# Optimization experiments

Measured on AMD Instinct MI355X. Metric: run time of the kernel, lower is better.

## Reference

```python
import jax, jax.numpy as jnp
import numpy as np

N_NODES = 50000
N_EDGES = 600000
CH = 128      # units / channels
RBF = 200     # ceil(cutoff/gap) = ceil(20.0/0.1)
LOG2 = 0.6931471805599453


def shifted_softplus(x):
    # tf.where(x < 14, softplus(where(x < 14, x, 0)), x) - log(2)
    safe = jnp.where(x < 14.0, x, jnp.zeros_like(x))
    return jnp.where(x < 14.0, jax.nn.softplus(safe), x) - LOG2


def _glorot(key, shape):
    fan_in = shape[0] if len(shape) > 1 else shape[0]
    fan_out = shape[-1]
    lim = np.sqrt(6.0 / (fan_in + fan_out))
    return jax.random.uniform(key, shape, jnp.float32, -lim, lim)


def setup_inputs() -> dict:
    key = jax.random.key(0)
    ks = jax.random.split(key, 12)
    rbf = jax.random.uniform(ks[0], (N_EDGES, RBF), jnp.float32)
    x = jax.random.normal(ks[1], (N_NODES, CH), jnp.float32)
    src = jax.random.randint(ks[2], (N_EDGES,), 0, N_NODES, jnp.int32)
    return {
        "rbf": rbf,
        "x": x,
        "src": src,
        "w1": _glorot(ks[3], (RBF, CH)),
        "b1": _glorot(ks[4], (CH,)),
        "w2": _glorot(ks[5], (CH, CH)),
        "b2": _glorot(ks[6], (CH,)),
        "w3": _glorot(ks[7], (CH, CH)),
        "w4": _glorot(ks[8], (CH, CH)),
        "b4": _glorot(ks[9], (CH,)),
        "w5": _glorot(ks[10], (CH, CH)),
        "b5": _glorot(ks[11], (CH,)),
    }


def reference(rbf, x, src, w1, b1, w2, b2, w3, w4, b4, w5, b5):
    # filter-generating MLP on edge RBF features: [E, RBF] -> [E, CH]
    h = shifted_softplus(rbf @ w1 + b1)
    w = shifted_softplus(h @ w2 + b2)
    # node feature transform, gather to edges by SOURCE index
    f = x @ w3                         # [N, CH]
    wf = w * f[src]                    # [E, CH] broadcast_node_to_edges + multiply
    # scatter-sum edges back to SOURCE nodes
    conv = jax.ops.segment_sum(wf, src, num_segments=N_NODES)  # [N, CH]
    # output MLP + residual
    y = shifted_softplus(conv @ w4 + b4)
    v = y @ w5 + b5
    return x + v
```

## Files before the change

### kernel.cpp

```cpp
#include <hip/hip_runtime.h>

#define CH      128
#define RBFD    200
#define NNODES  50000
#define NEDGES  600000
#define LOG2F_  0.6931471805599453f
#define K1P     224

typedef __attribute__((ext_vector_type(8))) __bf16 bf16x8;
typedef __attribute__((ext_vector_type(4))) float  f32x4;

__device__ __forceinline__ float ssp(float x) {
    float sp = (x < 14.0f) ? __logf(1.0f + __expf(x)) : x;
    return sp - LOG2F_;
}

__device__ __forceinline__ unsigned short f2bf(float f) {
    union { float f; unsigned int u; } v; v.f = f;
    unsigned int r = v.u + 0x7FFFu + ((v.u >> 16) & 1u);
    return (unsigned short)(r >> 16);
}

__device__ __forceinline__ float bf2f(unsigned short s) {
    union { unsigned int u; float f; } v; v.u = ((unsigned int)s) << 16;
    return v.f;
}

__device__ __forceinline__ bf16x8 load_cvt8(const float* p) {
    float4 f0 = *(const float4*)p;
    float4 f1 = *(const float4*)(p + 4);
    union { unsigned int u[4]; bf16x8 v; } r;
    asm("v_cvt_pk_bf16_f32 %0, %1, %2" : "=v"(r.u[0]) : "v"(f0.x), "v"(f0.y));
    asm("v_cvt_pk_bf16_f32 %0, %1, %2" : "=v"(r.u[1]) : "v"(f0.z), "v"(f0.w));
    asm("v_cvt_pk_bf16_f32 %0, %1, %2" : "=v"(r.u[2]) : "v"(f1.x), "v"(f1.y));
    asm("v_cvt_pk_bf16_f32 %0, %1, %2" : "=v"(r.u[3]) : "v"(f1.z), "v"(f1.w));
    return r.v;
}

__global__ __launch_bounds__(256) void prep_weights(const float* __restrict__ w1,
                                                    const float* __restrict__ w2,
                                                    unsigned short* __restrict__ w1T,
                                                    unsigned short* __restrict__ w2T) {
    int i = blockIdx.x * 256 + threadIdx.x;
    if (i < 128 * K1P) {
        int n = i / K1P, k = i % K1P;
        w1T[i] = (k < RBFD) ? f2bf(w1[k * CH + n]) : (unsigned short)0;
    } else {
        int j = i - 128 * K1P;
        if (j < 128 * 128) {
            int n = j / 128, k = j % 128;
            w2T[j] = f2bf(w2[k * CH + n]);
        }
    }
}

__global__ __launch_bounds__(256) void k_hist(const int* __restrict__ src, int* __restrict__ cur) {
    int e = blockIdx.x * 256 + threadIdx.x;
    if (e < NEDGES) atomicAdd(&cur[src[e]], 1);
}

__global__ __launch_bounds__(256) void k_scan1(const int* __restrict__ cur, int* __restrict__ bsum) {
    __shared__ int s[256];
    const int t = threadIdx.x;
    int i = blockIdx.x * 256 + t;
    s[t] = (i < NNODES) ? cur[i] : 0;
    __syncthreads();
    for (int d = 128; d > 0; d >>= 1) {
        if (t < d) s[t] += s[t + d];
        __syncthreads();
    }
    if (t == 0) bsum[blockIdx.x] = s[0];
}

__global__ __launch_bounds__(256) void k_scan2(const int* __restrict__ bsum, int* __restrict__ bpre) {
    __shared__ int s[256];
    const int t = threadIdx.x;
    int v0 = (t < 196) ? bsum[t] : 0;
    s[t] = v0;
    __syncthreads();
    for (int d = 1; d < 256; d <<= 1) {
        int v = (t >= d) ? s[t - d] : 0;
        __syncthreads();
        s[t] += v;
        __syncthreads();
    }
    if (t < 196) bpre[t] = s[t] - v0;
}

__global__ __launch_bounds__(256) void k_scan3(const int* __restrict__ deg_in,
                                               const int* __restrict__ bpre,
                                               int* __restrict__ csr_off,
                                               int* __restrict__ cur) {
    __shared__ int s[256];
    const int t = threadIdx.x, b = blockIdx.x;
    const int i = b * 256 + t;
    int d0 = (i < NNODES) ? deg_in[i] : 0;
    s[t] = d0;
    __syncthreads();
    for (int d = 1; d < 256; d <<= 1) {
        int v = (t >= d) ? s[t - d] : 0;
        __syncthreads();
        s[t] += v;
        __syncthreads();
    }
    if (i < NNODES) {
        int ex = bpre[b] + s[t] - d0;
        csr_off[i] = ex;
        cur[i] = ex;
    }
    if (i == NNODES - 1) csr_off[NNODES] = NEDGES;
}

__global__ __launch_bounds__(256) void k_fill(const int* __restrict__ src,
                                              int* __restrict__ cur,
                                              int* __restrict__ eidx) {
    int e = blockIdx.x * 256 + threadIdx.x;
    if (e < NEDGES) {
        int pos = atomicAdd(&cur[src[e]], 1);
        eidx[pos] = e;
    }
}

__global__ __launch_bounds__(256, 4) void edge_kernel2(const float* __restrict__ rbf,
                                                       const float* __restrict__ b1v,
                                                       const float* __restrict__ b2v,
                                                       const unsigned short* __restrict__ w1T,
                                                       const unsigned short* __restrict__ w2T,
                                                       unsigned short* __restrict__ wbuf) {
    __shared__ unsigned short tile[4][16 * 128];
    const int t = threadIdx.x;
    const int lane = t & 63;
    const int wv = t >> 6;
    const int l15 = lane & 15;
    const int lg  = lane >> 4;
    const size_t erow0 = (size_t)blockIdx.x * 64 + (size_t)wv * 16;
    unsigned short* my = tile[wv];
    char* myb = (char*)my;

    bf16x8 a1[7];
    const float* arow = rbf + (erow0 + l15) * RBFD;
#pragma unroll
    for (int kt = 0; kt < 6; kt++)
        a1[kt] = load_cvt8(arow + kt * 32 + lg * 8);
    if (lg == 0) {
        a1[6] = load_cvt8(arow + 192);
    } else {
        union { unsigned int u[4]; bf16x8 v; } z;
        z.u[0] = z.u[1] = z.u[2] = z.u[3] = 0;
        a1[6] = z.v;
    }

    const int myrow0 = lg * 4;

#pragma unroll
    for (int nt = 0; nt < 8; nt++) {
        f32x4 acc = {0.f, 0.f, 0.f, 0.f};
        const unsigned short* bbase = w1T + (size_t)(nt * 16 + l15) * K1P + lg * 8;
#pragma unroll
        for (int kt = 0; kt < 7; kt++) {
            bf16x8 b = *(const bf16x8*)(bbase + kt * 32);
            acc = __builtin_amdgcn_mfma_f32_16x16x32_bf16(a1[kt], b, acc, 0, 0, 0);
        }
        const float bias = b1v[nt * 16 + l15];
#pragma unroll
        for (int r = 0; r < 4; r++) {
            const int row = myrow0 + r;
            const int colb = (nt * 32 + l15 * 2) ^ ((row & 7) << 4);
            *(unsigned short*)(myb + row * 256 + colb) = f2bf(ssp(acc[r] + bias));
        }
    }

    bf16x8 a2[4];
#pragma unroll
    for (int kt = 0; kt < 4; kt++) {
        const int boff = l15 * 256 + ((kt * 64 + lg * 16) ^ ((l15 & 7) << 4));
        a2[kt] = *(const bf16x8*)(myb + boff);
    }

#pragma unroll
    for (int nt = 0; nt < 8; nt++) {
        f32x4 acc = {0.f, 0.f, 0.f, 0.f};
        const unsigned short* bbase = w2T + (size_t)(nt * 16 + l15) * 128 + lg * 8;
#pragma unroll
        for (int kt = 0; kt < 4; kt++) {
            bf16x8 b = *(const bf16x8*)(bbase + kt * 32);
            acc = __builtin_amdgcn_mfma_f32_16x16x32_bf16(a2[kt], b, acc, 0, 0, 0);
        }
        const float bias = b2v[nt * 16 + l15];
#pragma unroll
        for (int r = 0; r < 4; r++) {
            const int row = myrow0 + r;
            const int colb = (nt * 32 + l15 * 2) ^ ((row & 7) << 4);
            *(unsigned short*)(myb + row * 256 + colb) = f2bf(ssp(acc[r] + bias));
        }
    }

    {
        const int row = lane >> 2, q = lane & 3;
        float4 o[4];
#pragma unroll
        for (int j = 0; j < 4; j++) {
            const int boff = row * 256 + ((q * 64 + j * 16) ^ ((row & 7) << 4));
            o[j] = *(const float4*)(myb + boff);
        }
        float4* gdst = (float4*)((char*)wbuf + (erow0 + row) * 256 + q * 64);
#pragma unroll
        for (int j = 0; j < 4; j++) gdst[j] = o[j];
    }
}

__global__ __launch_bounds__(256) void node_gather2(const float* __restrict__ x,
                                                    const float* __restrict__ w3,
                                                    const float* __restrict__ w4,
                                                    const float* __restrict__ b4,
                                                    const float* __restrict__ w5,
                                                    const float* __restrict__ b5,
                                                    const unsigned short* __restrict__ wbuf,
                                                    const int* __restrict__ eidx,
                                                    const int* __restrict__ csr_off,
                                                    float* __restrict__ out,
                                                    int n_nodes) {
    __shared__ float A[32 * 128];
    __shared__ float B[32 * 128];
    const int t = threadIdx.x;
    const int n0 = blockIdx.x * 32;
    const int rows = min(32, n_nodes - n0);

    {
        const float4* g = (const float4*)(x + (size_t)n0 * CH);
        float4* s = (float4*)A;
        for (int i = t; i < rows * 32; i += 256) s[i] = g[i];
    }
    __syncthreads();

    const int c = t & 127, eh = t >> 7;
    float acc[16];

#pragma unroll
    for (int i = 0; i < 16; i++) acc[i] = 0.f;
    for (int k = 0; k < 128; k += 4) {
        const float wa = w3[(k + 0) * CH + c];
        const float wb = w3[(k + 1) * CH + c];
        const float wc = w3[(k + 2) * CH + c];
        const float wd = w3[(k + 3) * CH + c];
#pragma unroll
        for (int i = 0; i < 16; i++) {
            const float4 v = *(const float4*)&A[(eh * 16 + i) * CH + k];
            acc[i] = fmaf(v.x, wa, acc[i]);
            acc[i] = fmaf(v.y, wb, acc[i]);
            acc[i] = fmaf(v.z, wc, acc[i]);
            acc[i] = fmaf(v.w, wd, acc[i]);
        }
    }
#pragma unroll
    for (int i = 0; i < 16; i++) B[(eh * 16 + i) * 128 + c] = acc[i];
    __syncthreads();

    {
        const int lane = t & 63, wv = t >> 6;
        const int c0 = lane * 2;
        for (int rr = 0; rr < 8; rr++) {
            const int r = wv * 8 + rr;
            const int n = n0 + r;
            float s0 = 0.f, s1 = 0.f;
            if (n < n_nodes) {
                const int o0 = csr_off[n], o1 = csr_off[n + 1];
                int j = o0;
                for (; j + 3 < o1; j += 4) {
                    const int ea = eidx[j], eb = eidx[j + 1], ec = eidx[j + 2], ed = eidx[j + 3];
                    const unsigned ua = *(const unsigned*)(wbuf + (size_t)ea * CH + c0);
                    const unsigned ub = *(const unsigned*)(wbuf + (size_t)eb * CH + c0);
                    const unsigned uc = *(const unsigned*)(wbuf + (size_t)ec * CH + c0);
                    const unsigned ud = *(const unsigned*)(wbuf + (size_t)ed * CH + c0);
                    s0 += bf2f((unsigned short)ua) + bf2f((unsigned short)ub)
                        + bf2f((unsigned short)uc) + bf2f((unsigned short)ud);
                    s1 += bf2f((unsigned short)(ua >> 16)) + bf2f((unsigned short)(ub >> 16))
                        + bf2f((unsigned short)(uc >> 16)) + bf2f((unsigned short)(ud >> 16));
                }
                for (; j < o1; j++) {
                    const unsigned ua = *(const unsigned*)(wbuf + (size_t)eidx[j] * CH + c0);
                    s0 += bf2f((unsigned short)ua);
                    s1 += bf2f((unsigned short)(ua >> 16));
                }
            }
            const float2 f2 = *(const float2*)&B[r * 128 + c0];
            float2 v2;
            v2.x = (n < n_nodes) ? f2.x * s0 : 0.f;
            v2.y = (n < n_nodes) ? f2.y * s1 : 0.f;
            *(float2*)&B[r * 128 + c0] = v2;
        }
    }
    __syncthreads();

#pragma unroll
    for (int i = 0; i < 16; i++) acc[i] = 0.f;
    for (int k = 0; k < 128; k += 4) {
        const float wa = w4[(k + 0) * CH + c];
        const float wb = w4[(k + 1) * CH + c];
        const float wc = w4[(k + 2) * CH + c];
        const float wd = w4[(k + 3) * CH + c];
#pragma unroll
        for (int i = 0; i < 16; i++) {
            const float4 v = *(const float4*)&B[(eh * 16 + i) * CH + k];
            acc[i] = fmaf(v.x, wa, acc[i]);
            acc[i] = fmaf(v.y, wb, acc[i]);
            acc[i] = fmaf(v.z, wc, acc[i]);
            acc[i] = fmaf(v.w, wd, acc[i]);
        }
    }
    {
        const float bias4 = b4[c];
#pragma unroll
        for (int i = 0; i < 16; i++)
            A[(eh * 16 + i) * 128 + c] = ssp(acc[i] + bias4);
    }
    __syncthreads();

#pragma unroll
    for (int i = 0; i < 16; i++) acc[i] = 0.f;
    for (int k = 0; k < 128; k += 4) {
        const float wa = w5[(k + 0) * CH + c];
        const float wb = w5[(k + 1) * CH + c];
        const float wc = w5[(k + 2) * CH + c];
        const float wd = w5[(k + 3) * CH + c];
#pragma unroll
        for (int i = 0; i < 16; i++) {
            const float4 v = *(const float4*)&A[(eh * 16 + i) * CH + k];
            acc[i] = fmaf(v.x, wa, acc[i]);
            acc[i] = fmaf(v.y, wb, acc[i]);
            acc[i] = fmaf(v.z, wc, acc[i]);
            acc[i] = fmaf(v.w, wd, acc[i]);
        }
    }
    {
        const float bias5 = b5[c];
#pragma unroll
        for (int i = 0; i < 16; i++) {
            const int r = eh * 16 + i;
            if (r < rows) {
                const size_t off = ((size_t)(n0 + r)) * CH + c;
                out[off] = x[off] + acc[i] + bias5;
            }
        }
    }
}

static inline size_t align_up(size_t v, size_t a) { return (v + a - 1) & ~(a - 1); }

extern "C" void kernel_launch(void* const* d_in, const int* in_sizes, int n_in,
                              void* d_out, int out_size, void* d_ws, size_t ws_size,
                              hipStream_t stream) {
    const float* rbf = (const float*)d_in[0];
    const float* x   = (const float*)d_in[1];
    const int*   src = (const int*)d_in[2];
    const float* w1  = (const float*)d_in[3];
    const float* b1  = (const float*)d_in[4];
    const float* w2  = (const float*)d_in[5];
    const float* b2  = (const float*)d_in[6];
    const float* w3  = (const float*)d_in[7];
    const float* w4  = (const float*)d_in[8];
    const float* b4  = (const float*)d_in[9];
    const float* w5  = (const float*)d_in[10];
    const float* b5  = (const float*)d_in[11];

    float* out = (float*)d_out;
    const size_t wElems = 128 * K1P + 128 * 128;

    size_t off = 0;
    const size_t o_wbuf = off;  off = align_up(off + (size_t)NEDGES * CH * 2, 256);
    const size_t o_eidx = off;  off = align_up(off + (size_t)NEDGES * 4, 256);
    const size_t o_csr  = off;  off = align_up(off + (size_t)(NNODES + 1) * 4, 256);
    const size_t o_cur  = off;  off = align_up(off + (size_t)NNODES * 4, 256);
    const size_t o_bs   = off;  off = align_up(off + 256 * 4, 256);
    const size_t o_bp   = off;  off = align_up(off + 256 * 4, 256);
    const size_t o_wT   = off;  off = align_up(off + wElems * 2, 256);

    unsigned short* wbuf = (unsigned short*)((char*)d_ws + o_wbuf);
    int* eidx            = (int*)((char*)d_ws + o_eidx);
    int* csr_off         = (int*)((char*)d_ws + o_csr);
    int* cur             = (int*)((char*)d_ws + o_cur);
    int* bsum            = (int*)((char*)d_ws + o_bs);
    int* bpre            = (int*)((char*)d_ws + o_bp);
    unsigned short* w1T  = (unsigned short*)((char*)d_ws + o_wT);
    unsigned short* w2T  = w1T + 128 * K1P;

    hipMemsetAsync(cur, 0, (size_t)NNODES * 4, stream);
    prep_weights<<<(int)((wElems + 255) / 256), 256, 0, stream>>>(w1, w2, w1T, w2T);
    edge_kernel2<<<NEDGES / 64, 256, 0, stream>>>(rbf, b1, b2, w1T, w2T, wbuf);
    k_hist<<<(NEDGES + 255) / 256, 256, 0, stream>>>(src, cur);
    k_scan1<<<196, 256, 0, stream>>>(cur, bsum);
    k_scan2<<<1, 256, 0, stream>>>(bsum, bpre);
    k_scan3<<<196, 256, 0, stream>>>(cur, bpre, csr_off, cur);
    k_fill<<<(NEDGES + 255) / 256, 256, 0, stream>>>(src, cur, eidx);
    node_gather2<<<(NNODES + 31) / 32, 256, 0, stream>>>(x, w3, w4, b4, w5, b5,
                                                         wbuf, eidx, csr_off, out, NNODES);
}
```

Baseline: 593.0 us.

## Make edge MLP kernel persistent with weights staged in LDS

Rewrites the edge filter MLP as a persistent kernel of 256 blocks with 1024 threads. Each block copies padded bf16 W1/W2 (stride 232/136 to avoid bank conflicts) into shared memory once, then its waves pull 16-edge tiles through an atomic work counter. Weight B-operands come from LDS instead of global/L2, and biases are hoisted into registers. It also switches to a branchless softplus and uses the hardware bf16 convert instruction. The costs are a large LDS footprint (about 60 KB for weights plus 64 KB for tiles), which limits occupancy to one block per CU, and contention on the atomic counter.

```diff
diff --git a/kernel.cpp b/kernel.cpp
--- a/kernel.cpp
+++ b/kernel.cpp
@@ -4,14 +4,22 @@
 #define RBFD    200
 #define NNODES  50000
 #define NEDGES  600000
+#define NTILES  (NEDGES / 16)
 #define LOG2F_  0.6931471805599453f
-#define K1P     224
+
+#define W1STR   232
+#define W2STR   136
+#define W1ELEMS (128 * W1STR)
+#define W2ELEMS (128 * W2STR)
+#define WTOT    (W1ELEMS + W2ELEMS)
 
 typedef __attribute__((ext_vector_type(8))) __bf16 bf16x8;
 typedef __attribute__((ext_vector_type(4))) float  f32x4;
 
 __device__ __forceinline__ float ssp(float x) {
-    float sp = (x < 14.0f) ? __logf(1.0f + __expf(x)) : x;
+    float e  = __expf(x);
+    float sp = __logf(1.0f + e);
+    sp = (x < 14.0f) ? sp : x;
     return sp - LOG2F_;
 }
 
@@ -24,6 +32,12 @@
 __device__ __forceinline__ float bf2f(unsigned short s) {
     union { unsigned int u; float f; } v; v.u = ((unsigned int)s) << 16;
     return v.f;
+}
+
+__device__ __forceinline__ unsigned short cvt1bf(float f) {
+    unsigned int u;
+    asm("v_cvt_pk_bf16_f32 %0, %1, %2" : "=v"(u) : "v"(f), "v"(f));
+    return (unsigned short)u;
 }
 
 __device__ __forceinline__ bf16x8 load_cvt8(const float* p) {
@@ -39,18 +53,15 @@
 
 __global__ __launch_bounds__(256) void prep_weights(const float* __restrict__ w1,
                                                     const float* __restrict__ w2,
-                                                    unsigned short* __restrict__ w1T,
-                                                    unsigned short* __restrict__ w2T) {
+                                                    unsigned short* __restrict__ wp) {
     int i = blockIdx.x * 256 + threadIdx.x;
-    if (i < 128 * K1P) {
-        int n = i / K1P, k = i % K1P;
-        w1T[i] = (k < RBFD) ? f2bf(w1[k * CH + n]) : (unsigned short)0;
-    } else {
-        int j = i - 128 * K1P;
-        if (j < 128 * 128) {
-            int n = j / 128, k = j % 128;
-            w2T[j] = f2bf(w2[k * CH + n]);
-        }
+    if (i < W1ELEMS) {
+        int n = i / W1STR, k = i % W1STR;
+        wp[i] = (k < RBFD) ? f2bf(w1[k * CH + n]) : (unsigned short)0;
+    } else if (i < WTOT) {
+        int j = i - W1ELEMS;
+        int n = j / W2STR, k = j % W2STR;
+        wp[i] = (k < CH) ? f2bf(w2[k * CH + n]) : (unsigned short)0;
     }
 }
 
@@ -121,91 +132,112 @@
     }
 }
 
-__global__ __launch_bounds__(256, 4) void edge_kernel2(const float* __restrict__ rbf,
-                                                       const float* __restrict__ b1v,
-                                                       const float* __restrict__ b2v,
-                                                       const unsigned short* __restrict__ w1T,
-                                                       const unsigned short* __restrict__ w2T,
-                                                       unsigned short* __restrict__ wbuf) {
-    __shared__ unsigned short tile[4][16 * 128];
+__global__ __launch_bounds__(1024, 4) void edge_kernel3(const float* __restrict__ rbf,
+                                                        const float* __restrict__ b1v,
+                                                        const float* __restrict__ b2v,
+                                                        const unsigned short* __restrict__ wp,
+                                                        unsigned short* __restrict__ wbuf,
+                                                        int* __restrict__ ctr) {
+    __shared__ unsigned short wsh[WTOT];
+    __shared__ unsigned short htile[16 * 16 * 128];
     const int t = threadIdx.x;
     const int lane = t & 63;
-    const int wv = t >> 6;
+    const int wvid = t >> 6;
     const int l15 = lane & 15;
     const int lg  = lane >> 4;
-    const size_t erow0 = (size_t)blockIdx.x * 64 + (size_t)wv * 16;
-    unsigned short* my = tile[wv];
-    char* myb = (char*)my;
-
-    bf16x8 a1[7];
-    const float* arow = rbf + (erow0 + l15) * RBFD;
-#pragma unroll
-    for (int kt = 0; kt < 6; kt++)
-        a1[kt] = load_cvt8(arow + kt * 32 + lg * 8);
-    if (lg == 0) {
-        a1[6] = load_cvt8(arow + 192);
-    } else {
-        union { unsigned int u[4]; bf16x8 v; } z;
-        z.u[0] = z.u[1] = z.u[2] = z.u[3] = 0;
-        a1[6] = z.v;
-    }
-
+
+    {
+        const float4* g = (const float4*)wp;
+        float4* s = (float4*)wsh;
+        for (int i = t; i < WTOT / 8; i += 1024) s[i] = g[i];
+    }
+
+    float bias1[8], bias2[8];
+#pragma unroll
+    for (int nt = 0; nt < 8; nt++) {
+        bias1[nt] = b1v[nt * 16 + l15];
+        bias2[nt] = b2v[nt * 16 + l15];
+    }
+    __syncthreads();
+
+    const unsigned short* w1s = wsh;
+    const unsigned short* w2s = wsh + W1ELEMS;
+    char* myb = (char*)(htile + wvid * (16 * 128));
     const int myrow0 = lg * 4;
 
-#pragma unroll
-    for (int nt = 0; nt < 8; nt++) {
-        f32x4 acc = {0.f, 0.f, 0.f, 0.f};
-        const unsigned short* bbase = w1T + (size_t)(nt * 16 + l15) * K1P + lg * 8;
-#pragma unroll
-        for (int kt = 0; kt < 7; kt++) {
-            bf16x8 b = *(const bf16x8*)(bbase + kt * 32);
-            acc = __builtin_amdgcn_mfma_f32_16x16x32_bf16(a1[kt], b, acc, 0, 0, 0);
-        }
-        const float bias = b1v[nt * 16 + l15];
-#pragma unroll
-        for (int r = 0; r < 4; r++) {
-            const int row = myrow0 + r;
-            const int colb = (nt * 32 + l15 * 2) ^ ((row & 7) << 4);
-            *(unsigned short*)(myb + row * 256 + colb) = f2bf(ssp(acc[r] + bias));
-        }
-    }
-
-    bf16x8 a2[4];
-#pragma unroll
-    for (int kt = 0; kt < 4; kt++) {
-        const int boff = l15 * 256 + ((kt * 64 + lg * 16) ^ ((l15 & 7) << 4));
-        a2[kt] = *(const bf16x8*)(myb + boff);
-    }
-
-#pragma unroll
-    for (int nt = 0; nt < 8; nt++) {
-        f32x4 acc = {0.f, 0.f, 0.f, 0.f};
-        const unsigned short* bbase = w2T + (size_t)(nt * 16 + l15) * 128 + lg * 8;
+    while (true) {
+        int tile;
+        if (lane == 0) tile = atomicAdd(ctr, 1);
+        tile = __shfl(tile, 0);
+        if (tile >= NTILES) break;
+        const size_t erow0 = (size_t)tile * 16;
+
+        bf16x8 a1[7];
+        const float* arow = rbf + (erow0 + l15) * RBFD;
+#pragma unroll
+        for (int kt = 0; kt < 6; kt++)
+            a1[kt] = load_cvt8(arow + kt * 32 + lg * 8);
+        if (lg == 0) {
+            a1[6] = load_cvt8(arow + 192);
+        } else {
+            union { unsigned int u[4]; bf16x8 v; } z;
+            z.u[0] = z.u[1] = z.u[2] = z.u[3] = 0;
+            a1[6] = z.v;
+        }
+
+#pragma unroll
+        for (int nt = 0; nt < 8; nt++) {
+            f32x4 acc = {0.f, 0.f, 0.f, 0.f};
+            const unsigned short* bbase = w1s + (nt * 16 + l15) * W1STR + lg * 8;
+#pragma unroll
+            for (int kt = 0; kt < 7; kt++) {
+                bf16x8 b = *(const bf16x8*)(bbase + kt * 32);
+                acc = __builtin_amdgcn_mfma_f32_16x16x32_bf16(a1[kt], b, acc, 0, 0, 0);
+            }
+#pragma unroll
+            for (int r = 0; r < 4; r++) {
+                const int row = myrow0 + r;
+                const int colb = (nt * 32 + l15 * 2) ^ ((row & 7) << 4);
+                *(unsigned short*)(myb + row * 256 + colb) = cvt1bf(ssp(acc[r] + bias1[nt]));
+            }
+        }
+
+        bf16x8 a2[4];
 #pragma unroll
         for (int kt = 0; kt < 4; kt++) {
-            bf16x8 b = *(const bf16x8*)(bbase + kt * 32);
-            acc = __builtin_amdgcn_mfma_f32_16x16x32_bf16(a2[kt], b, acc, 0, 0, 0);
-        }
-        const float bias = b2v[nt * 16 + l15];
-#pragma unroll
-        for (int r = 0; r < 4; r++) {
-            const int row = myrow0 + r;
-            const int colb = (nt * 32 + l15 * 2) ^ ((row & 7) << 4);
-            *(unsigned short*)(myb + row * 256 + colb) = f2bf(ssp(acc[r] + bias));
-        }
-    }
-
-    {
-        const int row = lane >> 2, q = lane & 3;
-        float4 o[4];
-#pragma unroll
-        for (int j = 0; j < 4; j++) {
-            const int boff = row * 256 + ((q * 64 + j * 16) ^ ((row & 7) << 4));
-            o[j] = *(const float4*)(myb + boff);
-        }
-        float4* gdst = (float4*)((char*)wbuf + (erow0 + row) * 256 + q * 64);
-#pragma unroll
-        for (int j = 0; j < 4; j++) gdst[j] = o[j];
+            const int boff = l15 * 256 + ((kt * 64 + lg * 16) ^ ((l15 & 7) << 4));
+            a2[kt] = *(const bf16x8*)(myb + boff);
+        }
+
+#pragma unroll
+        for (int nt = 0; nt < 8; nt++) {
+            f32x4 acc = {0.f, 0.f, 0.f, 0.f};
+            const unsigned short* bbase = w2s + (nt * 16 + l15) * W2STR + lg * 8;
+#pragma unroll
+            for (int kt = 0; kt < 4; kt++) {
+                bf16x8 b = *(const bf16x8*)(bbase + kt * 32);
+                acc = __builtin_amdgcn_mfma_f32_16x16x32_bf16(a2[kt], b, acc, 0, 0, 0);
+            }
+#pragma unroll
+            for (int r = 0; r < 4; r++) {
+                const int row = myrow0 + r;
+                const int colb = (nt * 32 + l15 * 2) ^ ((row & 7) << 4);
+                *(unsigned short*)(myb + row * 256 + colb) = cvt1bf(ssp(acc[r] + bias2[nt]));
+            }
+        }
+
+        {
+            const int row = lane >> 2, q = lane & 3;
+            float4 o[4];
+#pragma unroll
+            for (int j = 0; j < 4; j++) {
+                const int boff = row * 256 + ((q * 64 + j * 16) ^ ((row & 7) << 4));
+                o[j] = *(const float4*)(myb + boff);
+            }
+            float4* gdst = (float4*)((char*)wbuf + (erow0 + row) * 256 + q * 64);
+#pragma unroll
+            for (int j = 0; j < 4; j++) gdst[j] = o[j];
+        }
     }
 }
 
@@ -364,7 +396,6 @@
     const float* b5  = (const float*)d_in[11];
 
     float* out = (float*)d_out;
-    const size_t wElems = 128 * K1P + 128 * 128;
 
     size_t off = 0;
     const size_t o_wbuf = off;  off = align_up(off + (size_t)NEDGES * CH * 2, 256);
@@ -373,7 +404,8 @@
     const size_t o_cur  = off;  off = align_up(off + (size_t)NNODES * 4, 256);
     const size_t o_bs   = off;  off = align_up(off + 256 * 4, 256);
     const size_t o_bp   = off;  off = align_up(off + 256 * 4, 256);
-    const size_t o_wT   = off;  off = align_up(off + wElems * 2, 256);
+    const size_t o_wp   = off;  off = align_up(off + (size_t)WTOT * 2, 256);
+    const size_t o_ctr  = off;  off = align_up(off + 256, 256);
 
     unsigned short* wbuf = (unsigned short*)((char*)d_ws + o_wbuf);
     int* eidx            = (int*)((char*)d_ws + o_eidx);
@@ -381,12 +413,13 @@
     int* cur             = (int*)((char*)d_ws + o_cur);
     int* bsum            = (int*)((char*)d_ws + o_bs);
     int* bpre            = (int*)((char*)d_ws + o_bp);
-    unsigned short* w1T  = (unsigned short*)((char*)d_ws + o_wT);
-    unsigned short* w2T  = w1T + 128 * K1P;
+    unsigned short* wp   = (unsigned short*)((char*)d_ws + o_wp);
+    int* ctr             = (int*)((char*)d_ws + o_ctr);
 
     hipMemsetAsync(cur, 0, (size_t)NNODES * 4, stream);
-    prep_weights<<<(int)((wElems + 255) / 256), 256, 0, stream>>>(w1, w2, w1T, w2T);
-    edge_kernel2<<<NEDGES / 64, 256, 0, stream>>>(rbf, b1, b2, w1T, w2T, wbuf);
+    hipMemsetAsync(ctr, 0, 4, stream);
+    prep_weights<<<(WTOT + 255) / 256, 256, 0, stream>>>(w1, w2, wp);
+    edge_kernel3<<<256, 1024, 0, stream>>>(rbf, b1, b2, wp, wbuf, ctr);
     k_hist<<<(NEDGES + 255) / 256, 256, 0, stream>>>(src, cur);
     k_scan1<<<196, 256, 0, stream>>>(cur, bsum);
     k_scan2<<<1, 256, 0, stream>>>(bsum, bpre);
```

Result: slower. 769.2 us (+29.7%).
